# Optimization experiments

Measured on AMD Instinct MI355X. Metric: run time of the kernel, lower is better.

The kernel has to match this reference:

```python
import jax, jax.numpy as jnp
import numpy as np

MAX_SEQ = 512
HIDDEN = 1024
E = 2 * HIDDEN  # expansion
S = 128         # head dim s
EPS = 1e-5


def setup_inputs() -> dict:
    key = jax.random.key(0)
    ks = jax.random.split(key, 10)
    B, N = 32, 512
    x = jax.random.normal(ks[0], (B, N, HIDDEN), dtype=jnp.float32)
    attention_mask = jnp.ones((B, N), dtype=jnp.float32)
    gamma = jax.random.uniform(ks[1], (2, S), dtype=jnp.float32)
    beta = jax.random.uniform(ks[2], (2, S), dtype=jnp.float32)
    w = jax.random.uniform(ks[3], (2 * MAX_SEQ - 1,), dtype=jnp.float32)
    a_p = jax.random.uniform(ks[4], (1, S), dtype=jnp.float32)
    b_p = jax.random.uniform(ks[5], (1, S), dtype=jnp.float32)
    # uv: Linear(hidden -> 2e+s), stored input-major for x @ uv_w
    uv_w = jax.random.normal(ks[6], (HIDDEN, 2 * E + S), dtype=jnp.float32) * 0.02
    uv_b = jnp.zeros((2 * E + S,), dtype=jnp.float32)
    o_w = jax.random.normal(ks[7], (E, HIDDEN), dtype=jnp.float32) * 0.02
    o_b = jnp.zeros((HIDDEN,), dtype=jnp.float32)
    ln_g = jnp.ones((HIDDEN,), dtype=jnp.float32)
    ln_b = jnp.zeros((HIDDEN,), dtype=jnp.float32)
    return {"x": x, "attention_mask": attention_mask, "gamma": gamma, "beta": beta,
            "w": w, "a_p": a_p, "b_p": b_p, "uv_w": uv_w, "uv_b": uv_b,
            "o_w": o_w, "o_b": o_b, "ln_g": ln_g, "ln_b": ln_b}


def _rope_seq(x):
    # x: [b, n, 2, s]; rotary positions along axis 1 (matches module's rope(x, dim=1))
    n, d = x.shape[1], x.shape[-1]
    half = d // 2
    pos = jnp.arange(n, dtype=jnp.float32)
    # inv_freq = 10000 ** (arange(half)/half)  (freq_seq = -arange/half, inv = 10000**-freq_seq)
    inv_freq = jnp.power(10000.0, jnp.arange(half, dtype=jnp.float32) / half)
    sinusoid = pos[:, None] * inv_freq  # [n, half]
    sin = jnp.sin(sinusoid)[None, :, None, :]
    cos = jnp.cos(sinusoid)[None, :, None, :]
    x1, x2 = jnp.split(x, 2, axis=-1)
    return jnp.concatenate([x1 * cos - x2 * sin, x2 * cos + x1 * sin], axis=-1)


def _rel_pos_bias(w, seq_len):
    # Toeplitz trick (max_seq_length <= 512 path)
    t = jnp.pad(w[: 2 * MAX_SEQ - 1], (0, MAX_SEQ))          # [3S-1]
    t = jnp.tile(t, MAX_SEQ)[: -MAX_SEQ].reshape(-1, MAX_SEQ, 3 * MAX_SEQ - 2)
    r = (2 * MAX_SEQ - 1) // 2
    t = t[..., r:-r]                                          # [1, S, S]
    return t[:, :seq_len, :seq_len]


def reference(x, attention_mask, gamma, beta, w, a_p, b_p, uv_w, uv_b, o_w, o_b, ln_g, ln_b):
    n = x.shape[1]
    shortcut = x
    mu = jnp.mean(x, axis=-1, keepdims=True)
    var = jnp.mean(jnp.square(x - mu), axis=-1, keepdims=True)
    xn = (x - mu) * jax.lax.rsqrt(var + EPS) * ln_g + ln_b
    uv = jax.nn.silu(xn @ uv_w + uv_b)                        # [b, n, 2e+s]
    u, v, base = jnp.split(uv, [E, 2 * E], axis=-1)
    base = base[..., None, :] * gamma + beta                  # [b, n, 2, s]
    base = _rope_seq(base)
    q, k = base[:, :, 0], base[:, :, 1]                       # [b, n, s]
    qk = jnp.einsum('bnd,bmd->bnm', q, k)
    qk = qk + ((1.0 - attention_mask) * -1e12)[:, None, :]
    bias = _rel_pos_bias(w, n)                                # [1, n, n]
    kernel = jnp.square(jax.nn.relu(qk / MAX_SEQ + bias))
    out = u * jnp.einsum('bnm,bme->bne', kernel, v)           # [b, n, e]
    return out @ o_w + o_b + shortcut
```

## Files before the change

kernel.cpp:

```cpp
#include <hip/hip_runtime.h>
#include <math.h>

#define HIDDEN 1024
#define NSEQ   512
#define BATCH  32
#define EDIM   2048
#define SDIM   128
#define UVN    (2 * EDIM + SDIM)

using short8  = __attribute__((ext_vector_type(8))) short;
using float4x = __attribute__((ext_vector_type(4))) float;

__device__ __forceinline__ ushort f2bf(float f) {
    unsigned u = __float_as_uint(f);
    u += 0x7FFFu + ((u >> 16) & 1u);
    return (ushort)(u >> 16);
}
__device__ __forceinline__ float bf2f(ushort h) {
    return __uint_as_float(((unsigned)h) << 16);
}

#define ASYNC16(gp, lp) __builtin_amdgcn_global_load_lds( \
    (const __attribute__((address_space(1))) unsigned int*)(unsigned long long)(const void*)(gp), \
    (__attribute__((address_space(3))) unsigned int*)(unsigned int)(unsigned long long)(const void*)(lp), \
    16, 0, 0)

__global__ __launch_bounds__(64) void tab_kernel(float* __restrict__ sin_t,
                                                 float* __restrict__ cos_t) {
    int i = blockIdx.x;
    int j = threadIdx.x;
    double inv = pow(10000.0, (double)j / 64.0);
    double ang = (double)i * inv;
    sin_t[i * 64 + j] = (float)sin(ang);
    cos_t[i * 64 + j] = (float)cos(ang);
}

__global__ __launch_bounds__(256) void transpose_f32_bf16(const float* __restrict__ src,
                                                          ushort* __restrict__ dst,
                                                          int R, int Cc) {
    __shared__ float tile[32][33];
    const int bx = blockIdx.x;
    const int by = blockIdx.y;
    const int lx = threadIdx.x & 31;
    const int gy = threadIdx.x >> 5;
#pragma unroll
    for (int i = 0; i < 4; ++i) {
        int r = by * 32 + gy + i * 8;
        tile[gy + i * 8][lx] = src[(size_t)r * Cc + bx * 32 + lx];
    }
    __syncthreads();
#pragma unroll
    for (int i = 0; i < 4; ++i) {
        int c = bx * 32 + gy + i * 8;
        dst[(size_t)c * R + by * 32 + lx] = f2bf(tile[lx][gy + i * 8]);
    }
}

__global__ __launch_bounds__(256) void ln_kernel(const float* __restrict__ x,
                                                 const float* __restrict__ g,
                                                 const float* __restrict__ b,
                                                 ushort* __restrict__ xn) {
    const size_t t = blockIdx.x;
    const int tid = threadIdx.x;
    const float4 v = ((const float4*)(x + t * HIDDEN))[tid];
    float s = v.x + v.y + v.z + v.w;
#pragma unroll
    for (int off = 32; off > 0; off >>= 1) s += __shfl_down(s, off);
    __shared__ float red[4];
    const int wid = tid >> 6, lane = tid & 63;
    if (lane == 0) red[wid] = s;
    __syncthreads();
    const float mean = (red[0] + red[1] + red[2] + red[3]) * (1.0f / HIDDEN);
    __syncthreads();
    const float dx = v.x - mean, dy = v.y - mean, dz = v.z - mean, dw = v.w - mean;
    float s2 = dx * dx + dy * dy + dz * dz + dw * dw;
#pragma unroll
    for (int off = 32; off > 0; off >>= 1) s2 += __shfl_down(s2, off);
    if (lane == 0) red[wid] = s2;
    __syncthreads();
    const float var = (red[0] + red[1] + red[2] + red[3]) * (1.0f / HIDDEN);
    const float rs = rsqrtf(var + 1e-5f);
    const float4 gv = ((const float4*)g)[tid];
    const float4 bv = ((const float4*)b)[tid];
    ushort4 o;
    o.x = f2bf(dx * rs * gv.x + bv.x);
    o.y = f2bf(dy * rs * gv.y + bv.y);
    o.z = f2bf(dz * rs * gv.z + bv.z);
    o.w = f2bf(dw * rs * gv.w + bv.w);
    ((ushort4*)(xn + t * HIDDEN))[tid] = o;
}

__device__ __forceinline__ void mfma_core_128(const ushort* __restrict__ A,
                                              const ushort* __restrict__ Bt,
                                              const int lda, const int ldb, const int K,
                                              const int m0, const int n0,
                                              ushort* As, ushort* Bs,
                                              float4x (&acc)[4][4]) {
    const int tid = threadIdx.x;
    const int l = tid & 63, w = tid >> 6;
    const int wm = (w & 1) << 6, wn = (w >> 1) << 6;

    const int c0 = w * 128 + l;
    const int r0 = c0 >> 2, kc0 = (c0 & 3) * 8;
    const int c1 = c0 + 64;
    const int r1 = c1 >> 2, kc1 = (c1 & 3) * 8;
    char* ldsA0 = (char*)As + (size_t)(w * 128) * 16;
    char* ldsA1 = ldsA0 + 1024;
    char* ldsB0 = (char*)Bs + (size_t)(w * 128) * 16;
    char* ldsB1 = ldsB0 + 1024;
    const ushort* gA0 = A + (size_t)(m0 + r0) * lda + kc0;
    const ushort* gA1 = A + (size_t)(m0 + r1) * lda + kc1;
    const ushort* gB0 = Bt + (size_t)(n0 + r0) * ldb + kc0;
    const ushort* gB1 = Bt + (size_t)(n0 + r1) * ldb + kc1;

    const int lr = l & 15, lk = (l >> 4) * 8;
    int aoff[4], boff[4];
#pragma unroll
    for (int i = 0; i < 4; ++i) {
        aoff[i] = (wm + i * 16 + lr) * 32 + lk;
        boff[i] = (wn + i * 16 + lr) * 32 + lk;
    }

    for (int k0 = 0; k0 < K; k0 += 32) {
        __syncthreads();
        ASYNC16(gA0 + k0, ldsA0);
        ASYNC16(gA1 + k0, ldsA1);
        ASYNC16(gB0 + k0, ldsB0);
        ASYNC16(gB1 + k0, ldsB1);
        __syncthreads();
        short8 af[4], bfr[4];
#pragma unroll
        for (int i = 0; i < 4; ++i) af[i] = *(const short8*)(As + aoff[i]);
#pragma unroll
        for (int i = 0; i < 4; ++i) bfr[i] = *(const short8*)(Bs + boff[i]);
#pragma unroll
        for (int mi = 0; mi < 4; ++mi)
#pragma unroll
            for (int ni = 0; ni < 4; ++ni)
                acc[mi][ni] = __builtin_amdgcn_mfma_f32_16x16x32_bf16(
                    af[mi], bfr[ni], acc[mi][ni], 0, 0, 0);
    }
}

template <typename F>
__device__ __forceinline__ void epilogue_loop(const float4x (&acc)[4][4],
                                              int m0, int n0, F body) {
    const int l = threadIdx.x & 63, w = threadIdx.x >> 6;
    const int wm = (w & 1) << 6, wn = (w >> 1) << 6;
    const int lrow = (l >> 4) << 2, lcol = l & 15;
#pragma unroll
    for (int mi = 0; mi < 4; ++mi)
#pragma unroll
        for (int ni = 0; ni < 4; ++ni)
#pragma unroll
            for (int r = 0; r < 4; ++r) {
                const int m = m0 + wm + mi * 16 + lrow + r;
                const int n = n0 + wn + ni * 16 + lcol;
                body(m, n, acc[mi][ni][r]);
            }
}

__device__ __forceinline__ void mfma_core_256(const ushort* __restrict__ A,
                                              const ushort* __restrict__ Bt,
                                              const int lda, const int ldb, const int K,
                                              const int m0, const int n0,
                                              char* smem,
                                              float4x (&acc)[8][4]) {
    const int tid = threadIdx.x;
    const int l = tid & 63, w = tid >> 6;
    const int wm = w >> 2, wn = w & 3;

    const int srow = l >> 2;
    const int kcol = (w & 1) * 32 + (((tid & 3) ^ ((l >> 3) & 3)) << 3);
    const int rb0  = w >> 1;
    const ushort* gA[4];
    const ushort* gB[4];
#pragma unroll
    for (int j = 0; j < 4; ++j) {
        const int row = (j * 4 + rb0) * 16 + srow;
        gA[j] = A  + (size_t)(m0 + row) * lda + kcol;
        gB[j] = Bt + (size_t)(n0 + row) * ldb + kcol;
    }
    char* const ldsA = smem;
    char* const ldsB = smem + 65536;
    const int wdst = w * 1024;

#define STG_A(buf, j, t)  ASYNC16(gA[j] + (size_t)(t) * 64, ldsA + (buf) * 32768 + (j) * 8192 + wdst)
#define STG_B(buf, j, t)  ASYNC16(gB[j] + (size_t)(t) * 64, ldsB + (buf) * 32768 + (j) * 8192 + wdst)
#define RAWBAR() do { __builtin_amdgcn_sched_barrier(0); __builtin_amdgcn_s_barrier(); \
                      __builtin_amdgcn_sched_barrier(0); } while (0)
#define WAITV(N) asm volatile("s_waitcnt vmcnt(" #N ")" ::: "memory")

    const int LB = (l & 15) * 64 + (((l >> 4) ^ ((l >> 1) & 3)) << 4);
    const int rbbA0 = wm * 4;
    const int rbbA1 = 8 + wm * 4;
    const int cbbB0 = wn * 2;
    const int cbbB1 = 8 + wn * 2;

    const int KT = K >> 6;

    STG_A(0, 0, 0); STG_A(0, 1, 0);
    STG_B(0, 0, 0); STG_B(0, 1, 0);
    STG_B(0, 2, 0); STG_B(0, 3, 0);
    STG_A(0, 2, 0); STG_A(0, 3, 0);
    STG_A(1, 0, 1); STG_A(1, 1, 1);
    STG_B(1, 0, 1); STG_B(1, 1, 1);
    STG_B(1, 2, 1); STG_B(1, 3, 1);
    WAITV(10);
    RAWBAR();

    for (int t = 0; t < KT; ++t) {
        const int buf = t & 1, nbuf = buf ^ 1;
        const char* Ab = ldsA + buf * 32768;
        const char* Bb = ldsB + buf * 32768;
        short8 a[4][2], b0[2][2], b1[2][2];

#pragma unroll
        for (int mi = 0; mi < 4; ++mi) {
            a[mi][0] = *(const short8*)(Ab + (rbbA0 + mi) * 2048 + LB);
            a[mi][1] = *(const short8*)(Ab + (rbbA0 + mi) * 2048 + 1024 + LB);
        }
#pragma unroll
        for (int ni = 0; ni < 2; ++ni) {
            b0[ni][0] = *(const short8*)(Bb + (cbbB0 + ni) * 2048 + LB);
            b0[ni][1] = *(const short8*)(Bb + (cbbB0 + ni) * 2048 + 1024 + LB);
        }
        if (t + 1 < KT) { STG_A(nbuf, 2, t + 1); STG_A(nbuf, 3, t + 1); }
        RAWBAR();
        __builtin_amdgcn_s_setprio(1);
#pragma unroll
        for (int mi = 0; mi < 4; ++mi)
#pragma unroll
            for (int ni = 0; ni < 2; ++ni) {
                acc[mi][ni] = __builtin_amdgcn_mfma_f32_16x16x32_bf16(a[mi][0], b0[ni][0], acc[mi][ni], 0, 0, 0);
                acc[mi][ni] = __builtin_amdgcn_mfma_f32_16x16x32_bf16(a[mi][1], b0[ni][1], acc[mi][ni], 0, 0, 0);
            }
        __builtin_amdgcn_s_setprio(0);
        if (t < KT - 1) { WAITV(10); } else { WAITV(2); }
        RAWBAR();

#pragma unroll
        for (int ni = 0; ni < 2; ++ni) {
            b1[ni][0] = *(const short8*)(Bb + (cbbB1 + ni) * 2048 + LB);
            b1[ni][1] = *(const short8*)(Bb + (cbbB1 + ni) * 2048 + 1024 + LB);
        }
        if (t + 2 < KT) { STG_A(buf, 0, t + 2); STG_A(buf, 1, t + 2); }
        RAWBAR();
        __builtin_amdgcn_s_setprio(1);
#pragma unroll
        for (int mi = 0; mi < 4; ++mi)
#pragma unroll
            for (int ni = 0; ni < 2; ++ni) {
                acc[mi][2 + ni] = __builtin_amdgcn_mfma_f32_16x16x32_bf16(a[mi][0], b1[ni][0], acc[mi][2 + ni], 0, 0, 0);
                acc[mi][2 + ni] = __builtin_amdgcn_mfma_f32_16x16x32_bf16(a[mi][1], b1[ni][1], acc[mi][2 + ni], 0, 0, 0);
            }
        __builtin_amdgcn_s_setprio(0);
        if (t < KT - 2) { WAITV(10); } else if (t == KT - 2) { WAITV(8); } else { WAITV(0); }
        RAWBAR();

#pragma unroll
        for (int mi = 0; mi < 4; ++mi) {
            a[mi][0] = *(const short8*)(Ab + (rbbA1 + mi) * 2048 + LB);
            a[mi][1] = *(const short8*)(Ab + (rbbA1 + mi) * 2048 + 1024 + LB);
        }
        if (t + 2 < KT) {
            STG_B(buf, 0, t + 2); STG_B(buf, 1, t + 2);
            STG_B(buf, 2, t + 2); STG_B(buf, 3, t + 2);
        }
        RAWBAR();
        __builtin_amdgcn_s_setprio(1);
#pragma unroll
        for (int mi = 0; mi < 4; ++mi)
#pragma unroll
            for (int ni = 0; ni < 2; ++ni) {
                acc[4 + mi][2 + ni] = __builtin_amdgcn_mfma_f32_16x16x32_bf16(a[mi][0], b1[ni][0], acc[4 + mi][2 + ni], 0, 0, 0);
                acc[4 + mi][2 + ni] = __builtin_amdgcn_mfma_f32_16x16x32_bf16(a[mi][1], b1[ni][1], acc[4 + mi][2 + ni], 0, 0, 0);
            }
#pragma unroll
        for (int mi = 0; mi < 4; ++mi)
#pragma unroll
            for (int ni = 0; ni < 2; ++ni) {
                acc[4 + mi][ni] = __builtin_amdgcn_mfma_f32_16x16x32_bf16(a[mi][0], b0[ni][0], acc[4 + mi][ni], 0, 0, 0);
                acc[4 + mi][ni] = __builtin_amdgcn_mfma_f32_16x16x32_bf16(a[mi][1], b0[ni][1], acc[4 + mi][ni], 0, 0, 0);
            }
        __builtin_amdgcn_s_setprio(0);
        if (t < KT - 2) { WAITV(10); } else if (t == KT - 2) { WAITV(4); }
        RAWBAR();
    }
#undef STG_A
#undef STG_B
#undef RAWBAR
#undef WAITV
}

template <typename F>
__device__ __forceinline__ void epilogue_256(const float4x (&acc)[8][4],
                                             int m0, int n0, F body) {
    const int tid = threadIdx.x;
    const int l = tid & 63, w = tid >> 6;
    const int wm = w >> 2, wn = w & 3;
    const int lrow = (l >> 4) << 2, lcol = l & 15;
#pragma unroll
    for (int i = 0; i < 8; ++i)
#pragma unroll
        for (int j = 0; j < 4; ++j)
#pragma unroll
            for (int r = 0; r < 4; ++r) {
                const int m = m0 + (i >> 2) * 128 + wm * 64 + (i & 3) * 16 + lrow + r;
                const int n = n0 + (j >> 1) * 128 + wn * 32 + (j & 1) * 16 + lcol;
                body(m, n, acc[i][j][r]);
            }
}

__global__ __launch_bounds__(512) void gemm_uv2(const ushort* __restrict__ A,
                                                const ushort* __restrict__ Bt,
                                                const float* __restrict__ bias,
                                                ushort* __restrict__ U,
                                                ushort* __restrict__ VT) {
    __shared__ __align__(16) char smem[131072];
    float4x acc[8][4] = {};
    const int n0 = blockIdx.x * 256, m0 = blockIdx.y * 256;
    mfma_core_256(A, Bt, HIDDEN, HIDDEN, HIDDEN, m0, n0, smem, acc);
    if (blockIdx.x < 8) {
        epilogue_256(acc, m0, n0, [&](int m, int n, float aval) {
            float val = aval + bias[n];
            val = val / (1.0f + expf(-val));
            U[(size_t)m * EDIM + n] = f2bf(val);
        });
    } else {
        epilogue_256(acc, m0, n0, [&](int m, int n, float aval) {
            float val = aval + bias[n];
            val = val / (1.0f + expf(-val));
            const int e = n - EDIM;
            const int b = m >> 9;
            const int s = m & (NSEQ - 1);
            VT[((size_t)b * EDIM + e) * NSEQ + s] = f2bf(val);
        });
    }
}

__global__ __launch_bounds__(256) void gemm_base_mfma(const ushort* __restrict__ A,
                                                      const ushort* __restrict__ Bt,
                                                      const float* __restrict__ bias,
                                                      float* __restrict__ BASE) {
    __shared__ ushort As[128 * 32], Bs[128 * 32];
    float4x acc[4][4] = {};
    const int n0 = 2 * EDIM;
    const int m0 = blockIdx.y * 128;
    mfma_core_128(A, Bt, HIDDEN, HIDDEN, HIDDEN, m0, n0, As, Bs, acc);
    epilogue_loop(acc, m0, n0, [&](int m, int n, float aval) {
        float val = aval + bias[n];
        val = val / (1.0f + expf(-val));
        BASE[(size_t)m * SDIM + (n - 2 * EDIM)] = val;
    });
}

__global__ __launch_bounds__(128) void rope_kernel(const float* __restrict__ base,
                                                   const float* __restrict__ gamma,
                                                   const float* __restrict__ beta,
                                                   const float* __restrict__ sin_t,
                                                   const float* __restrict__ cos_t,
                                                   float* __restrict__ q,
                                                   float* __restrict__ k) {
    const size_t t = blockIdx.x;
    const int d = threadIdx.x;
    const int pos = (int)(t & (NSEQ - 1));
    __shared__ float vq[128], vk[128];
    const float bval = base[t * SDIM + d];
    vq[d] = bval * gamma[d] + beta[d];
    vk[d] = bval * gamma[SDIM + d] + beta[SDIM + d];
    __syncthreads();
    const int h = d & 63;
    const float sn = sin_t[pos * 64 + h];
    const float cs = cos_t[pos * 64 + h];
    float oq, ok;
    if (d < 64) {
        oq = vq[d] * cs - vq[d + 64] * sn;
        ok = vk[d] * cs - vk[d + 64] * sn;
    } else {
        oq = vq[d] * cs + vq[d - 64] * sn;
        ok = vk[d] * cs + vk[d - 64] * sn;
    }
    q[t * SDIM + d] = oq;
    k[t * SDIM + d] = ok;
}

__global__ __launch_bounds__(256) void gemm_qk(const float* __restrict__ q,
                                               const float* __restrict__ k,
                                               const float* __restrict__ mask,
                                               const float* __restrict__ w,
                                               ushort* __restrict__ km) {
    __shared__ float As[16][68];
    __shared__ float Bs[16][68];
    const int b = blockIdx.z;
    const float* A = q + (size_t)b * NSEQ * SDIM;
    const float* B = k + (size_t)b * NSEQ * SDIM;
    const int tid = threadIdx.x;
    const int tx = tid & 15, ty = tid >> 4;
    const int arow = tid >> 2, acol = (tid & 3) << 2;
    const int n0 = blockIdx.x * 64, m0 = blockIdx.y * 64;
    float acc[4][4] = {};
    for (int k0 = 0; k0 < SDIM; k0 += 16) {
        float4 av = *(const float4*)(A + (size_t)(m0 + arow) * SDIM + (k0 + acol));
        float4 bv = *(const float4*)(B + (size_t)(n0 + arow) * SDIM + (k0 + acol));
        As[acol + 0][arow] = av.x; As[acol + 1][arow] = av.y;
        As[acol + 2][arow] = av.z; As[acol + 3][arow] = av.w;
        Bs[acol + 0][arow] = bv.x; Bs[acol + 1][arow] = bv.y;
        Bs[acol + 2][arow] = bv.z; Bs[acol + 3][arow] = bv.w;
        __syncthreads();
#pragma unroll
        for (int kk = 0; kk < 16; ++kk) {
            const float4 a4 = *(const float4*)&As[kk][ty << 2];
            const float4 b4 = *(const float4*)&Bs[kk][tx << 2];
            const float a[4] = {a4.x, a4.y, a4.z, a4.w};
            const float bbv[4] = {b4.x, b4.y, b4.z, b4.w};
#pragma unroll
            for (int i = 0; i < 4; ++i)
#pragma unroll
                for (int j = 0; j < 4; ++j)
                    acc[i][j] = fmaf(a[i], bbv[j], acc[i][j]);
        }
        __syncthreads();
    }
    const float inv512 = 1.0f / 512.0f;
#pragma unroll
    for (int i = 0; i < 4; ++i) {
        const int ii = m0 + (ty << 2) + i;
#pragma unroll
        for (int j = 0; j < 4; ++j) {
            const int jj = n0 + (tx << 2) + j;
            const float mterm = (1.0f - mask[b * NSEQ + jj]) * -1e12f;
            float val = (acc[i][j] + mterm) * inv512 + w[511 + jj - ii];
            val = fmaxf(val, 0.0f);
            km[(size_t)b * NSEQ * NSEQ + (size_t)ii * NSEQ + jj] = f2bf(val * val);
        }
    }
}

__global__ __launch_bounds__(512) void gemm_pv2(const ushort* __restrict__ km,
                                                const ushort* __restrict__ vT,
                                                ushort* __restrict__ ug) {
    __shared__ __align__(16) char smem[131072];
    float4x acc[8][4] = {};
    const int b = blockIdx.z;
    const int n0 = blockIdx.x * 256, m0 = blockIdx.y * 256;
    mfma_core_256(km + (size_t)b * NSEQ * NSEQ, vT + (size_t)b * EDIM * NSEQ,
                  NSEQ, NSEQ, NSEQ, m0, n0, smem, acc);
    const size_t tokbase = (size_t)b * NSEQ;
    epilogue_256(acc, m0, n0, [&](int m, int n, float aval) {
        const size_t idx = (tokbase + m) * EDIM + n;
        ug[idx] = f2bf(bf2f(ug[idx]) * aval);
    });
}

__global__ __launch_bounds__(512) void gemm_out2(const ushort* __restrict__ A,
                                                 const ushort* __restrict__ Bt,
                                                 const float* __restrict__ ob,
                                                 const float* __restrict__ x,
                                                 float* __restrict__ out) {
    __shared__ __align__(16) char smem[131072];
    float4x acc[8][4] = {};
    const int n0 = blockIdx.x * 256, m0 = blockIdx.y * 256;
    mfma_core_256(A, Bt, EDIM, EDIM, EDIM, m0, n0, smem, acc);
    epilogue_256(acc, m0, n0, [&](int m, int n, float aval) {
        out[(size_t)m * HIDDEN + n] = aval + ob[n] + x[(size_t)m * HIDDEN + n];
    });
}

extern "C" void kernel_launch(void* const* d_in, const int* in_sizes, int n_in,
                              void* d_out, int out_size, void* d_ws, size_t ws_size,
                              hipStream_t stream) {
    const float* x     = (const float*)d_in[0];
    const float* mask  = (const float*)d_in[1];
    const float* gamma = (const float*)d_in[2];
    const float* beta  = (const float*)d_in[3];
    const float* w     = (const float*)d_in[4];
    const float* uv_w  = (const float*)d_in[7];
    const float* uv_b  = (const float*)d_in[8];
    const float* o_w   = (const float*)d_in[9];
    const float* o_b   = (const float*)d_in[10];
    const float* ln_g  = (const float*)d_in[11];
    const float* ln_b  = (const float*)d_in[12];
    float* out = (float*)d_out;

    int C = 32;
    while (C > 1) {
        unsigned long long need = (unsigned long long)C * 5505024ull + 13107200ull;
        if (need <= (unsigned long long)ws_size) break;
        C >>= 1;
    }
    const int R = C * NSEQ;

    char* p = (char*)d_ws;
    ushort* xn  = (ushort*)p;  p += (size_t)C * 1048576;
    ushort* u   = (ushort*)p;  p += (size_t)C * 2097152;
    ushort* vT  = (ushort*)p;  p += (size_t)C * 2097152;
    float* base = (float*)p;   p += (size_t)C * 262144;
    float* sint = (float*)p;   p += 131072;
    float* cost = (float*)p;   p += 131072;
    ushort* uv_wt = (ushort*)p; p += 8650752;
    ushort* o_wt  = (ushort*)p; p += 4194304;
    float* q  = (float*)xn;
    float* k  = (float*)((char*)xn + (size_t)C * 262144);
    ushort* km = (ushort*)((char*)xn + (size_t)C * 524288);

    hipLaunchKernelGGL(tab_kernel, dim3(512), dim3(64), 0, stream, sint, cost);
    hipLaunchKernelGGL(transpose_f32_bf16, dim3(132, 32), dim3(256), 0, stream,
                       uv_w, uv_wt, HIDDEN, UVN);
    hipLaunchKernelGGL(transpose_f32_bf16, dim3(32, 64), dim3(256), 0, stream,
                       o_w, o_wt, EDIM, HIDDEN);

    for (int b0 = 0; b0 < BATCH; b0 += C) {
        const float* xc = x + (size_t)b0 * NSEQ * HIDDEN;
        float*       oc = out + (size_t)b0 * NSEQ * HIDDEN;
        const float* mc = mask + (size_t)b0 * NSEQ;
        hipLaunchKernelGGL(ln_kernel, dim3(R), dim3(256), 0, stream, xc, ln_g, ln_b, xn);
        hipLaunchKernelGGL(gemm_uv2, dim3(16, R / 256), dim3(512), 0, stream,
                           xn, uv_wt, uv_b, u, vT);
        hipLaunchKernelGGL(gemm_base_mfma, dim3(1, R / 128), dim3(256), 0, stream,
                           xn, uv_wt, uv_b, base);
        hipLaunchKernelGGL(rope_kernel, dim3(R), dim3(128), 0, stream,
                           base, gamma, beta, sint, cost, q, k);
        hipLaunchKernelGGL(gemm_qk, dim3(8, 8, C), dim3(256), 0, stream, q, k, mc, w, km);
        hipLaunchKernelGGL(gemm_pv2, dim3(8, 2, C), dim3(512), 0, stream, km, vT, u);
        hipLaunchKernelGGL(gemm_out2, dim3(4, R / 256), dim3(512), 0, stream,
                           u, o_wt, o_b, xc, oc);
    }
}
```

Before: 550.4 us.

## Use split-bf16 MFMA for QK and a 1024-thread UV GEMM core

The fp32 FMA QK^T GEMM becomes an MFMA kernel. Rope now emits q and k as hi/lo bf16 pairs, and three MFMA products (hh, hl, lh) approximate fp32 accuracy on the matrix cores. Separately, the UV projection GEMM moves to a new 1024-thread core with 16 waves, each holding a 4x4 accumulator tile, double-buffered async LDS loads and a simpler per-iteration sync. The QK path trades FMA throughput for extra MFMA passes and more global traffic for the hi/lo arrays. The UV change alters occupancy, register pressure and synchronisation cost.

```diff
diff --git a/kernel.cpp b/kernel.cpp
--- a/kernel.cpp
+++ b/kernel.cpp
@@ -210,7 +210,7 @@
     RAWBAR();
 
     for (int t = 0; t < KT; ++t) {
-        const int buf = t & 1, nbuf = buf ^ 1;
+        const int buf = t & 1;
         const char* Ab = ldsA + buf * 32768;
         const char* Bb = ldsB + buf * 32768;
         short8 a[4][2], b0[2][2], b1[2][2];
@@ -225,7 +225,7 @@
             b0[ni][0] = *(const short8*)(Bb + (cbbB0 + ni) * 2048 + LB);
             b0[ni][1] = *(const short8*)(Bb + (cbbB0 + ni) * 2048 + 1024 + LB);
         }
-        if (t + 1 < KT) { STG_A(nbuf, 2, t + 1); STG_A(nbuf, 3, t + 1); }
+        if (t + 1 < KT) { STG_A(buf ^ 1, 2, t + 1); STG_A(buf ^ 1, 3, t + 1); }
         RAWBAR();
         __builtin_amdgcn_s_setprio(1);
 #pragma unroll
@@ -312,23 +312,105 @@
             }
 }
 
-__global__ __launch_bounds__(512) void gemm_uv2(const ushort* __restrict__ A,
-                                                const ushort* __restrict__ Bt,
-                                                const float* __restrict__ bias,
-                                                ushort* __restrict__ U,
-                                                ushort* __restrict__ VT) {
+__device__ __forceinline__ void mfma_core_v3(const ushort* __restrict__ A,
+                                             const ushort* __restrict__ Bt,
+                                             const int lda, const int ldb, const int K,
+                                             const int m0, const int n0,
+                                             char* smem,
+                                             float4x (&acc)[4][4]) {
+    const int tid = threadIdx.x;
+    const int l = tid & 63, w = tid >> 6;
+    const int wm = w >> 2, wn = w & 3;
+
+    const int srow = l >> 2;
+    const int kswz = ((l & 3) ^ ((l >> 3) & 3)) << 3;
+    const ushort* gA = A + (size_t)(m0 + w * 16 + srow) * lda + kswz;
+    const ushort* gB = Bt + (size_t)(n0 + w * 16 + srow) * ldb + kswz;
+    char* const ldsA = smem;
+    char* const ldsB = smem + 65536;
+    const int woff = w * 2048;
+
+    const int LB = (l & 15) * 64 + (((l >> 4) ^ ((l >> 1) & 3)) << 4);
+    const int rbb = wm * 4, cbb = wn * 4;
+    const int KT = K >> 6;
+
+    ASYNC16(gA, ldsA + woff);
+    ASYNC16(gA + 32, ldsA + woff + 1024);
+    ASYNC16(gB, ldsB + woff);
+    ASYNC16(gB + 32, ldsB + woff + 1024);
+    __syncthreads();
+
+    for (int t = 0; t < KT; ++t) {
+        const int buf = t & 1;
+        const char* Ab = ldsA + buf * 32768;
+        const char* Bb = ldsB + buf * 32768;
+        if (t + 1 < KT) {
+            const size_t g = (size_t)(t + 1) * 64;
+            char* dA = ldsA + (buf ^ 1) * 32768 + woff;
+            char* dB = ldsB + (buf ^ 1) * 32768 + woff;
+            ASYNC16(gA + g, dA);
+            ASYNC16(gA + g + 32, dA + 1024);
+            ASYNC16(gB + g, dB);
+            ASYNC16(gB + g + 32, dB + 1024);
+        }
+        __builtin_amdgcn_sched_barrier(0);
+#pragma unroll
+        for (int kh = 0; kh < 2; ++kh) {
+            short8 a[4], b[4];
+#pragma unroll
+            for (int i = 0; i < 4; ++i) {
+                a[i] = *(const short8*)(Ab + (rbb + i) * 2048 + kh * 1024 + LB);
+                b[i] = *(const short8*)(Bb + (cbb + i) * 2048 + kh * 1024 + LB);
+            }
+            __builtin_amdgcn_s_setprio(1);
+#pragma unroll
+            for (int i = 0; i < 4; ++i)
+#pragma unroll
+                for (int j = 0; j < 4; ++j)
+                    acc[i][j] = __builtin_amdgcn_mfma_f32_16x16x32_bf16(
+                        a[i], b[j], acc[i][j], 0, 0, 0);
+            __builtin_amdgcn_s_setprio(0);
+        }
+        __syncthreads();
+    }
+}
+
+template <typename F>
+__device__ __forceinline__ void epilogue_v3(const float4x (&acc)[4][4],
+                                            int m0, int n0, F body) {
+    const int tid = threadIdx.x;
+    const int l = tid & 63, w = tid >> 6;
+    const int wm = w >> 2, wn = w & 3;
+    const int lrow = (l >> 4) << 2, lcol = l & 15;
+#pragma unroll
+    for (int i = 0; i < 4; ++i)
+#pragma unroll
+        for (int j = 0; j < 4; ++j)
+#pragma unroll
+            for (int r = 0; r < 4; ++r) {
+                const int m = m0 + wm * 64 + i * 16 + lrow + r;
+                const int n = n0 + wn * 64 + j * 16 + lcol;
+                body(m, n, acc[i][j][r]);
+            }
+}
+
+__global__ __launch_bounds__(1024, 4) void gemm_uv3(const ushort* __restrict__ A,
+                                                    const ushort* __restrict__ Bt,
+                                                    const float* __restrict__ bias,
+                                                    ushort* __restrict__ U,
+                                                    ushort* __restrict__ VT) {
     __shared__ __align__(16) char smem[131072];
-    float4x acc[8][4] = {};
+    float4x acc[4][4] = {};
     const int n0 = blockIdx.x * 256, m0 = blockIdx.y * 256;
-    mfma_core_256(A, Bt, HIDDEN, HIDDEN, HIDDEN, m0, n0, smem, acc);
+    mfma_core_v3(A, Bt, HIDDEN, HIDDEN, HIDDEN, m0, n0, smem, acc);
     if (blockIdx.x < 8) {
-        epilogue_256(acc, m0, n0, [&](int m, int n, float aval) {
+        epilogue_v3(acc, m0, n0, [&](int m, int n, float aval) {
             float val = aval + bias[n];
             val = val / (1.0f + expf(-val));
             U[(size_t)m * EDIM + n] = f2bf(val);
         });
     } else {
-        epilogue_256(acc, m0, n0, [&](int m, int n, float aval) {
+        epilogue_v3(acc, m0, n0, [&](int m, int n, float aval) {
             float val = aval + bias[n];
             val = val / (1.0f + expf(-val));
             const int e = n - EDIM;
@@ -360,8 +442,10 @@
                                                    const float* __restrict__ beta,
                                                    const float* __restrict__ sin_t,
                                                    const float* __restrict__ cos_t,
-                                                   float* __restrict__ q,
-                                                   float* __restrict__ k) {
+                                                   ushort* __restrict__ qh,
+                                                   ushort* __restrict__ ql,
+                                                   ushort* __restrict__ kh,
+                                                   ushort* __restrict__ kl) {
     const size_t t = blockIdx.x;
     const int d = threadIdx.x;
     const int pos = (int)(t & (NSEQ - 1));
@@ -381,60 +465,99 @@
         oq = vq[d] * cs + vq[d - 64] * sn;
         ok = vk[d] * cs + vk[d - 64] * sn;
     }
-    q[t * SDIM + d] = oq;
-    k[t * SDIM + d] = ok;
-}
-
-__global__ __launch_bounds__(256) void gemm_qk(const float* __restrict__ q,
-                                               const float* __restrict__ k,
-                                               const float* __restrict__ mask,
-                                               const float* __restrict__ w,
-                                               ushort* __restrict__ km) {
-    __shared__ float As[16][68];
-    __shared__ float Bs[16][68];
+    const ushort qhv = f2bf(oq);
+    const ushort khv = f2bf(ok);
+    qh[t * SDIM + d] = qhv;
+    ql[t * SDIM + d] = f2bf(oq - bf2f(qhv));
+    kh[t * SDIM + d] = khv;
+    kl[t * SDIM + d] = f2bf(ok - bf2f(khv));
+}
+
+__global__ __launch_bounds__(256, 4) void gemm_qk3(const ushort* __restrict__ qh,
+                                                   const ushort* __restrict__ ql,
+                                                   const ushort* __restrict__ kh,
+                                                   const ushort* __restrict__ kl,
+                                                   const float* __restrict__ mask,
+                                                   const float* __restrict__ w,
+                                                   ushort* __restrict__ km) {
+    __shared__ __align__(16) char smem[32768];
+    float4x acc[4][4] = {};
     const int b = blockIdx.z;
-    const float* A = q + (size_t)b * NSEQ * SDIM;
-    const float* B = k + (size_t)b * NSEQ * SDIM;
     const int tid = threadIdx.x;
-    const int tx = tid & 15, ty = tid >> 4;
-    const int arow = tid >> 2, acol = (tid & 3) << 2;
-    const int n0 = blockIdx.x * 64, m0 = blockIdx.y * 64;
-    float acc[4][4] = {};
-    for (int k0 = 0; k0 < SDIM; k0 += 16) {
-        float4 av = *(const float4*)(A + (size_t)(m0 + arow) * SDIM + (k0 + acol));
-        float4 bv = *(const float4*)(B + (size_t)(n0 + arow) * SDIM + (k0 + acol));
-        As[acol + 0][arow] = av.x; As[acol + 1][arow] = av.y;
-        As[acol + 2][arow] = av.z; As[acol + 3][arow] = av.w;
-        Bs[acol + 0][arow] = bv.x; Bs[acol + 1][arow] = bv.y;
-        Bs[acol + 2][arow] = bv.z; Bs[acol + 3][arow] = bv.w;
+    const int l = tid & 63, wv = tid >> 6;
+    const int wm = wv & 1, wn = wv >> 1;
+    const int m0 = blockIdx.y * 128, n0 = blockIdx.x * 128;
+    const size_t boff = (size_t)b * NSEQ * SDIM;
+
+    const int srow = l >> 2;
+    const int kswz = ((l & 3) ^ ((l >> 3) & 3)) << 3;
+    const size_t r0 = (size_t)(m0 + wv * 16 + srow) * SDIM + kswz;
+    const size_t r1 = r0 + (size_t)64 * SDIM;
+    const size_t c0 = (size_t)(n0 + wv * 16 + srow) * SDIM + kswz;
+    const size_t c1 = c0 + (size_t)64 * SDIM;
+    const ushort* gqh = qh + boff;
+    const ushort* gql = ql + boff;
+    const ushort* gkh = kh + boff;
+    const ushort* gkl = kl + boff;
+
+    const int LB = (l & 15) * 64 + (((l >> 4) ^ ((l >> 1) & 3)) << 4);
+
+    for (int t = 0; t < 4; ++t) {
+        const int g = t * 32;
+        ASYNC16(gqh + r0 + g, smem + wv * 1024);
+        ASYNC16(gqh + r1 + g, smem + (4 + wv) * 1024);
+        ASYNC16(gql + r0 + g, smem + 8192 + wv * 1024);
+        ASYNC16(gql + r1 + g, smem + 8192 + (4 + wv) * 1024);
+        ASYNC16(gkh + c0 + g, smem + 16384 + wv * 1024);
+        ASYNC16(gkh + c1 + g, smem + 16384 + (4 + wv) * 1024);
+        ASYNC16(gkl + c0 + g, smem + 24576 + wv * 1024);
+        ASYNC16(gkl + c1 + g, smem + 24576 + (4 + wv) * 1024);
         __syncthreads();
-#pragma unroll
-        for (int kk = 0; kk < 16; ++kk) {
-            const float4 a4 = *(const float4*)&As[kk][ty << 2];
-            const float4 b4 = *(const float4*)&Bs[kk][tx << 2];
-            const float a[4] = {a4.x, a4.y, a4.z, a4.w};
-            const float bbv[4] = {b4.x, b4.y, b4.z, b4.w};
-#pragma unroll
-            for (int i = 0; i < 4; ++i)
-#pragma unroll
-                for (int j = 0; j < 4; ++j)
-                    acc[i][j] = fmaf(a[i], bbv[j], acc[i][j]);
-        }
-        __syncthreads();
-    }
+        short8 ah[4], bh[4], bl[4];
+#pragma unroll
+        for (int i = 0; i < 4; ++i) {
+            ah[i] = *(const short8*)(smem + (wm * 4 + i) * 1024 + LB);
+            bh[i] = *(const short8*)(smem + 16384 + (wn * 4 + i) * 1024 + LB);
+            bl[i] = *(const short8*)(smem + 24576 + (wn * 4 + i) * 1024 + LB);
+        }
+        __builtin_amdgcn_s_setprio(1);
+#pragma unroll
+        for (int i = 0; i < 4; ++i)
+#pragma unroll
+            for (int j = 0; j < 4; ++j) {
+                acc[i][j] = __builtin_amdgcn_mfma_f32_16x16x32_bf16(ah[i], bh[j], acc[i][j], 0, 0, 0);
+                acc[i][j] = __builtin_amdgcn_mfma_f32_16x16x32_bf16(ah[i], bl[j], acc[i][j], 0, 0, 0);
+            }
+        __builtin_amdgcn_s_setprio(0);
+        short8 al[4];
+#pragma unroll
+        for (int i = 0; i < 4; ++i)
+            al[i] = *(const short8*)(smem + 8192 + (wm * 4 + i) * 1024 + LB);
+        __builtin_amdgcn_s_setprio(1);
+#pragma unroll
+        for (int i = 0; i < 4; ++i)
+#pragma unroll
+            for (int j = 0; j < 4; ++j)
+                acc[i][j] = __builtin_amdgcn_mfma_f32_16x16x32_bf16(al[i], bh[j], acc[i][j], 0, 0, 0);
+        __builtin_amdgcn_s_setprio(0);
+        if (t < 3) __syncthreads();
+    }
+
+    const int lrow = (l >> 4) << 2, lcol = l & 15;
     const float inv512 = 1.0f / 512.0f;
 #pragma unroll
-    for (int i = 0; i < 4; ++i) {
-        const int ii = m0 + (ty << 2) + i;
-#pragma unroll
-        for (int j = 0; j < 4; ++j) {
-            const int jj = n0 + (tx << 2) + j;
-            const float mterm = (1.0f - mask[b * NSEQ + jj]) * -1e12f;
-            float val = (acc[i][j] + mterm) * inv512 + w[511 + jj - ii];
-            val = fmaxf(val, 0.0f);
-            km[(size_t)b * NSEQ * NSEQ + (size_t)ii * NSEQ + jj] = f2bf(val * val);
-        }
-    }
+    for (int i = 0; i < 4; ++i)
+#pragma unroll
+        for (int j = 0; j < 4; ++j)
+#pragma unroll
+            for (int r = 0; r < 4; ++r) {
+                const int m = m0 + wm * 64 + i * 16 + lrow + r;
+                const int n = n0 + wn * 64 + j * 16 + lcol;
+                const float mterm = (1.0f - mask[b * NSEQ + n]) * -1e12f;
+                float val = (acc[i][j][r] + mterm) * inv512 + w[511 + n - m];
+                val = fmaxf(val, 0.0f);
+                km[(size_t)b * NSEQ * NSEQ + (size_t)m * NSEQ + n] = f2bf(val * val);
+            }
 }
 
 __global__ __launch_bounds__(512) void gemm_pv2(const ushort* __restrict__ km,
@@ -500,8 +623,10 @@
     float* cost = (float*)p;   p += 131072;
     ushort* uv_wt = (ushort*)p; p += 8650752;
     ushort* o_wt  = (ushort*)p; p += 4194304;
-    float* q  = (float*)xn;
-    float* k  = (float*)((char*)xn + (size_t)C * 262144);
+    ushort* qh = (ushort*)xn;
+    ushort* ql = (ushort*)((char*)xn + (size_t)C * 131072);
+    ushort* kh = (ushort*)((char*)xn + (size_t)C * 262144);
+    ushort* kl = (ushort*)((char*)xn + (size_t)C * 393216);
     ushort* km = (ushort*)((char*)xn + (size_t)C * 524288);
 
     hipLaunchKernelGGL(tab_kernel, dim3(512), dim3(64), 0, stream, sint, cost);
@@ -515,13 +640,14 @@
         float*       oc = out + (size_t)b0 * NSEQ * HIDDEN;
         const float* mc = mask + (size_t)b0 * NSEQ;
         hipLaunchKernelGGL(ln_kernel, dim3(R), dim3(256), 0, stream, xc, ln_g, ln_b, xn);
-        hipLaunchKernelGGL(gemm_uv2, dim3(16, R / 256), dim3(512), 0, stream,
+        hipLaunchKernelGGL(gemm_uv3, dim3(16, R / 256), dim3(1024), 0, stream,
                            xn, uv_wt, uv_b, u, vT);
         hipLaunchKernelGGL(gemm_base_mfma, dim3(1, R / 128), dim3(256), 0, stream,
                            xn, uv_wt, uv_b, base);
         hipLaunchKernelGGL(rope_kernel, dim3(R), dim3(128), 0, stream,
-                           base, gamma, beta, sint, cost, q, k);
-        hipLaunchKernelGGL(gemm_qk, dim3(8, 8, C), dim3(256), 0, stream, q, k, mc, w, km);
+                           base, gamma, beta, sint, cost, qh, ql, kh, kl);
+        hipLaunchKernelGGL(gemm_qk3, dim3(4, 4, C), dim3(256), 0, stream,
+                           qh, ql, kh, kl, mc, w, km);
         hipLaunchKernelGGL(gemm_pv2, dim3(8, 2, C), dim3(512), 0, stream, km, vT, u);
         hipLaunchKernelGGL(gemm_out2, dim3(4, R / 256), dim3(512), 0, stream,
                            u, o_wt, o_b, xc, oc);
```

Result: faster. 518.2 us (-5.8%).
